# Performance work log

Hardware: AMD Instinct MI355X
Metric: run time of the kernel (lower is better)

## Reference

```python
import jax, jax.numpy as jnp
import numpy as np

B, C, H, W = 16, 512, 32, 32
HEADS = 8
GROUPS = 32
EPS = 1e-5


def setup_inputs() -> dict:
    key = jax.random.key(0)
    ks = jax.random.split(key, 6)
    x = jax.random.normal(ks[0], (B, C, H, W), dtype=jnp.float32)
    gn_scale = jnp.ones((C,), dtype=jnp.float32)
    gn_bias = jnp.zeros((C,), dtype=jnp.float32)
    # 1x1 convs stored as dense matrices [out, in]
    qkv_w = jax.random.normal(ks[1], (3 * C, C), dtype=jnp.float32) * (1.0 / np.sqrt(C))
    proj_w = jax.random.normal(ks[2], (C, C), dtype=jnp.float32) * (1.0 / np.sqrt(C))
    proj_b = jax.random.normal(ks[3], (C,), dtype=jnp.float32) * 0.01
    return {"x": x, "gn_scale": gn_scale, "gn_bias": gn_bias,
            "qkv_w": qkv_w, "proj_w": proj_w, "proj_b": proj_b}


def _forward(x, gn_scale, gn_bias, qkv_w, proj_w, proj_b):
    b, c, h, w = x.shape
    d = c // HEADS  # head dim
    n = h * w
    # GroupNorm over (channels_per_group, h, w)
    xg = x.reshape(b, GROUPS, c // GROUPS, h, w)
    mu = jnp.mean(xg, axis=(2, 3, 4), keepdims=True)
    var = jnp.var(xg, axis=(2, 3, 4), keepdims=True)
    xn = ((xg - mu) * jax.lax.rsqrt(var + EPS)).reshape(b, c, h, w)
    xn = xn * gn_scale[None, :, None, None] + gn_bias[None, :, None, None]
    # 1x1 conv QKV: [b, 3c, n]
    qkv = jnp.einsum('oc,bcn->bon', qkv_w, xn.reshape(b, c, n))
    # split order: (qkv, heads, d)
    qkv = qkv.reshape(b, 3, HEADS, d, n)
    q, k, v = qkv[:, 0], qkv[:, 1], qkv[:, 2]  # each [b, heads, d, n]
    k = jax.nn.softmax(k, axis=-1)
    att = jnp.einsum('bhdn,bhen->bhde', k, v)          # [b, heads, d, d]
    out = jnp.einsum('bhde,bhdn->bhen', att, q)        # [b, heads, d, n]
    out = out.reshape(b, c, h, w)
    # 1x1 proj conv with bias
    out = jnp.einsum('oc,bchw->bohw', proj_w, out) + proj_b[None, :, None, None]
    return out


def reference(x, gn_scale, gn_bias, qkv_w, proj_w, proj_b):
    return _forward(x, gn_scale, gn_bias, qkv_w, proj_w, proj_b)
```

## Files before the change

### kernel.cpp

```cpp
#include <hip/hip_runtime.h>
#include <cstdint>
#include <cstddef>

#define B_ 16
#define C_ 512
#define N_ 1024
#define HEADS_ 8
#define D_ 64
#define CPG_ 16

typedef __bf16 bf16;
typedef bf16 bf16x4 __attribute__((ext_vector_type(4)));
typedef bf16 bf16x8 __attribute__((ext_vector_type(8)));
typedef bf16 bf16x16 __attribute__((ext_vector_type(16)));
typedef float f32x4 __attribute__((ext_vector_type(4)));

__device__ __forceinline__ void gload16(void* lds, const void* g) {
    __builtin_amdgcn_global_load_lds(
        (__attribute__((address_space(1))) void*)(void*)g,
        (__attribute__((address_space(3))) void*)lds, 16, 0, 0);
}

__global__ __launch_bounds__(256) void f32_to_bf16_k(const float* __restrict__ s,
                                                     bf16* __restrict__ d, int n) {
    int i = (blockIdx.x * 256 + threadIdx.x) * 4;
    if (i < n) {
        f32x4 v = *(const f32x4*)(s + i);
        bf16x4 o = {(bf16)v[0], (bf16)v[1], (bf16)v[2], (bf16)v[3]};
        *(bf16x4*)(d + i) = o;
    }
}

__global__ __launch_bounds__(256) void gn_kernel(const float* __restrict__ x,
                                                 const float* __restrict__ gamma,
                                                 const float* __restrict__ beta,
                                                 bf16* __restrict__ xnT) {
    const int blk = blockIdx.x;
    const int b = blk >> 5, g = blk & 31;
    const int c0 = g * CPG_;
    const float* xb = x + ((size_t)b * C_ + c0) * N_;
    const int t = threadIdx.x;

    f32x4 vals[CPG_];
    float sum = 0.f, ssq = 0.f;
#pragma unroll
    for (int c = 0; c < CPG_; ++c) {
        f32x4 v = *(const f32x4*)(xb + c * N_ + t * 4);
        vals[c] = v;
#pragma unroll
        for (int j = 0; j < 4; ++j) { sum += v[j]; ssq += v[j] * v[j]; }
    }
#pragma unroll
    for (int off = 32; off >= 1; off >>= 1) {
        sum += __shfl_xor(sum, off);
        ssq += __shfl_xor(ssq, off);
    }
    __shared__ float red[2][4];
    const int wv = t >> 6, lane = t & 63;
    if (lane == 0) { red[0][wv] = sum; red[1][wv] = ssq; }
    __syncthreads();
    sum = red[0][0] + red[0][1] + red[0][2] + red[0][3];
    ssq = red[1][0] + red[1][1] + red[1][2] + red[1][3];
    const float inv = 1.f / (float)(CPG_ * N_);
    float mean = sum * inv;
    float var = ssq * inv - mean * mean;
    float rstd = rsqrtf(var + 1e-5f);
    float ga[CPG_], be[CPG_];
#pragma unroll
    for (int c = 0; c < CPG_; ++c) {
        float gm = gamma[c0 + c] * rstd;
        ga[c] = gm;
        be[c] = beta[c0 + c] - mean * gm;
    }
#pragma unroll
    for (int j = 0; j < 4; ++j) {
        int n = t * 4 + j;
        bf16x16 o;
#pragma unroll
        for (int c = 0; c < CPG_; ++c) o[c] = (bf16)(vals[c][j] * ga[c] + be[c]);
        *(bf16x16*)(xnT + ((size_t)b * N_ + n) * C_ + c0) = o;
    }
}

template <int EPI>
__global__ __launch_bounds__(256, 2) void gemm_bt(const bf16* __restrict__ A,
                                                  const bf16* __restrict__ Bt,
                                                  int M, int N, int K,
                                                  void* __restrict__ o0,
                                                  void* __restrict__ o1,
                                                  void* __restrict__ o2,
                                                  const float* __restrict__ bias) {
    __shared__ __align__(16) bf16 As[2][128][64];
    __shared__ __align__(16) bf16 Bs[2][128][64];
    const int t = threadIdx.x;
    const int lane = t & 63, wv = t >> 6;
    const int wr = wv >> 1, wc = wv & 1;
    const int bn = blockIdx.x, bm = blockIdx.y, b = blockIdx.z;
    const bf16* Ab = A + (size_t)bm * 128 * K;
    const bf16* Bb = Bt + ((size_t)b * N + (size_t)bn * 128) * K;

    f32x4 acc[4][4];
#pragma unroll
    for (int mi = 0; mi < 4; ++mi)
#pragma unroll
        for (int ni = 0; ni < 4; ++ni) acc[mi][ni] = f32x4{0.f, 0.f, 0.f, 0.f};

    const int nk = K >> 6;

    auto stage = [&](int buf, int kt) {
#pragma unroll
        for (int rnd = 0; rnd < 4; ++rnd) {
            int idx = rnd * 256 + t;
            int row = idx >> 3, pb = idx & 7;
            int srcb = pb ^ (row & 7);
            gload16((char*)&As[buf][0][0] + (size_t)idx * 16,
                    Ab + (size_t)row * K + kt * 64 + srcb * 8);
        }
#pragma unroll
        for (int rnd = 0; rnd < 4; ++rnd) {
            int idx = rnd * 256 + t;
            int row = idx >> 3, pb = idx & 7;
            int srcb = pb ^ (row & 7);
            gload16((char*)&Bs[buf][0][0] + (size_t)idx * 16,
                    Bb + (size_t)row * K + kt * 64 + srcb * 8);
        }
    };
    auto compute = [&](int buf) {
#pragma unroll
        for (int ks = 0; ks < 2; ++ks) {
            bf16x8 af[4], bfr[4];
#pragma unroll
            for (int mi = 0; mi < 4; ++mi) {
                int r = wr * 64 + mi * 16 + (lane & 15);
                int bi = (ks * 4 + (lane >> 4)) ^ (r & 7);
                af[mi] = *(const bf16x8*)&As[buf][r][bi * 8];
            }
#pragma unroll
            for (int ni = 0; ni < 4; ++ni) {
                int r = wc * 64 + ni * 16 + (lane & 15);
                int bi = (ks * 4 + (lane >> 4)) ^ (r & 7);
                bfr[ni] = *(const bf16x8*)&Bs[buf][r][bi * 8];
            }
#pragma unroll
            for (int mi = 0; mi < 4; ++mi)
#pragma unroll
                for (int ni = 0; ni < 4; ++ni)
                    acc[mi][ni] = __builtin_amdgcn_mfma_f32_16x16x32_bf16(
                        af[mi], bfr[ni], acc[mi][ni], 0, 0, 0);
        }
    };

    stage(0, 0);
    asm volatile("s_waitcnt vmcnt(0)" ::: "memory");
    __syncthreads();
    for (int kt = 0; kt < nk - 1; ++kt) {
        const int cur = kt & 1;
        stage(cur ^ 1, kt + 1);
        compute(cur);
        asm volatile("s_waitcnt vmcnt(0)" ::: "memory");
        __syncthreads();
    }
    compute((nk - 1) & 1);

    const int rowb = bm * 128 + wr * 64;
    const int colb = bn * 128 + wc * 64;
#pragma unroll
    for (int mi = 0; mi < 4; ++mi) {
#pragma unroll
        for (int ni = 0; ni < 4; ++ni) {
            int r0 = rowb + mi * 16 + (lane >> 4) * 4;
            int cc = colb + ni * 16 + (lane & 15);
            if constexpr (EPI == 0) {
                bf16* qT = (bf16*)o0;
                float* kf = (float*)o1;
                bf16* vb = (bf16*)o2;
                if (r0 < 512) {
                    int h = r0 >> 6, d = r0 & 63;
                    bf16x4 pk;
#pragma unroll
                    for (int j = 0; j < 4; ++j) pk[j] = (bf16)acc[mi][ni][j];
                    *(bf16x4*)(qT + (((size_t)b * HEADS_ + h) * N_ + cc) * D_ + d) = pk;
                } else if (r0 < 1024) {
                    int h = (r0 >> 6) - 8, d = r0 & 63;
                    float* kp = kf + (((size_t)b * HEADS_ + h) * D_ + d) * N_ + cc;
#pragma unroll
                    for (int j = 0; j < 4; ++j) kp[(size_t)j * N_] = acc[mi][ni][j];
                } else {
                    int h = (r0 >> 6) - 16, d = r0 & 63;
                    bf16* vp = vb + (((size_t)b * HEADS_ + h) * D_ + d) * N_ + cc;
#pragma unroll
                    for (int j = 0; j < 4; ++j) vp[(size_t)j * N_] = (bf16)acc[mi][ni][j];
                }
            } else {
                float* outp = (float*)o0;
#pragma unroll
                for (int j = 0; j < 4; ++j)
                    outp[((size_t)b * C_ + r0 + j) * N_ + cc] = acc[mi][ni][j] + bias[r0 + j];
            }
        }
    }
}

__global__ __launch_bounds__(256) void softmax_k(const float* __restrict__ kf,
                                                 bf16* __restrict__ ksm) {
    const int row = blockIdx.x * 4 + (threadIdx.x >> 6);
    const int lane = threadIdx.x & 63;
    const float* rp = kf + (size_t)row * N_;
    f32x4 v[4];
    float mx = -1e30f;
#pragma unroll
    for (int i = 0; i < 4; ++i) {
        v[i] = *(const f32x4*)(rp + (lane + 64 * i) * 4);
#pragma unroll
        for (int j = 0; j < 4; ++j) mx = fmaxf(mx, v[i][j]);
    }
#pragma unroll
    for (int off = 32; off >= 1; off >>= 1) mx = fmaxf(mx, __shfl_xor(mx, off));
    float s = 0.f;
#pragma unroll
    for (int i = 0; i < 4; ++i)
#pragma unroll
        for (int j = 0; j < 4; ++j) { v[i][j] = __expf(v[i][j] - mx); s += v[i][j]; }
#pragma unroll
    for (int off = 32; off >= 1; off >>= 1) s += __shfl_xor(s, off);
    float inv = 1.f / s;
    bf16* op = ksm + (size_t)row * N_;
#pragma unroll
    for (int i = 0; i < 4; ++i) {
        bf16x4 o;
#pragma unroll
        for (int j = 0; j < 4; ++j) o[j] = (bf16)(v[i][j] * inv);
        *(bf16x4*)(op + (lane + 64 * i) * 4) = o;
    }
}

__global__ __launch_bounds__(256) void attn_kernel(const bf16* __restrict__ ksm,
                                                   const bf16* __restrict__ vb,
                                                   const bf16* __restrict__ qT,
                                                   bf16* __restrict__ o2T) {
    __shared__ float attp[2][64][64];
    __shared__ __align__(16) bf16 attT[64][64];
    const int bh = blockIdx.x;
    const int b = bh >> 3, h = bh & 7;
    const int t = threadIdx.x, lane = t & 63, wv = t >> 6;
    const bf16* kb = ksm + (size_t)bh * D_ * N_;
    const bf16* vv = vb + (size_t)bh * D_ * N_;
    const bf16* qb = qT + (size_t)bh * N_ * D_;

    f32x4 acc[4][4];
#pragma unroll
    for (int mi = 0; mi < 4; ++mi)
#pragma unroll
        for (int ni = 0; ni < 4; ++ni) acc[mi][ni] = f32x4{0.f, 0.f, 0.f, 0.f};

    const int k0 = wv * 256;
    for (int kk = 0; kk < 256; kk += 32) {
        bf16x8 af[4], bfr[4];
#pragma unroll
        for (int mi = 0; mi < 4; ++mi)
            af[mi] = *(const bf16x8*)(kb + (size_t)(mi * 16 + (lane & 15)) * N_ + k0 + kk + (lane >> 4) * 8);
#pragma unroll
        for (int ni = 0; ni < 4; ++ni)
            bfr[ni] = *(const bf16x8*)(vv + (size_t)(ni * 16 + (lane & 15)) * N_ + k0 + kk + (lane >> 4) * 8);
#pragma unroll
        for (int mi = 0; mi < 4; ++mi)
#pragma unroll
            for (int ni = 0; ni < 4; ++ni)
                acc[mi][ni] = __builtin_amdgcn_mfma_f32_16x16x32_bf16(
                    af[mi], bfr[ni], acc[mi][ni], 0, 0, 0);
    }
    if (wv < 2) {
#pragma unroll
        for (int mi = 0; mi < 4; ++mi)
#pragma unroll
            for (int ni = 0; ni < 4; ++ni)
#pragma unroll
                for (int j = 0; j < 4; ++j)
                    attp[wv][mi * 16 + (lane >> 4) * 4 + j][ni * 16 + (lane & 15)] = acc[mi][ni][j];
    }
    __syncthreads();
    if (wv >= 2) {
#pragma unroll
        for (int mi = 0; mi < 4; ++mi)
#pragma unroll
            for (int ni = 0; ni < 4; ++ni)
#pragma unroll
                for (int j = 0; j < 4; ++j)
                    attp[wv - 2][mi * 16 + (lane >> 4) * 4 + j][ni * 16 + (lane & 15)] += acc[mi][ni][j];
    }
    __syncthreads();
    for (int i = t; i < 4096; i += 256) {
        int d = i >> 6, e = i & 63;
        float s = attp[0][d][e] + attp[1][d][e];
        attT[e][d ^ ((e & 7) << 3)] = (bf16)s;
    }
    __syncthreads();

    for (int nc = 0; nc < 4; ++nc) {
        int n0 = wv * 256 + nc * 64;
        f32x4 a2[4][4];
#pragma unroll
        for (int mi = 0; mi < 4; ++mi)
#pragma unroll
            for (int ni = 0; ni < 4; ++ni) a2[mi][ni] = f32x4{0.f, 0.f, 0.f, 0.f};
#pragma unroll
        for (int ks = 0; ks < 2; ++ks) {
            bf16x8 af[4], bfr[4];
#pragma unroll
            for (int mi = 0; mi < 4; ++mi) {
                int r = mi * 16 + (lane & 15);
                int cb = ks * 32 + (lane >> 4) * 8;
                af[mi] = *(const bf16x8*)&attT[r][cb ^ ((r & 7) << 3)];
            }
#pragma unroll
            for (int ni = 0; ni < 4; ++ni)
                bfr[ni] = *(const bf16x8*)(qb + (size_t)(n0 + ni * 16 + (lane & 15)) * D_ + ks * 32 + (lane >> 4) * 8);
#pragma unroll
            for (int mi = 0; mi < 4; ++mi)
#pragma unroll
                for (int ni = 0; ni < 4; ++ni)
                    a2[mi][ni] = __builtin_amdgcn_mfma_f32_16x16x32_bf16(
                        af[mi], bfr[ni], a2[mi][ni], 0, 0, 0);
        }
#pragma unroll
        for (int mi = 0; mi < 4; ++mi) {
#pragma unroll
            for (int ni = 0; ni < 4; ++ni) {
                int e0 = mi * 16 + (lane >> 4) * 4;
                int nn = n0 + ni * 16 + (lane & 15);
                bf16x4 pk;
#pragma unroll
                for (int j = 0; j < 4; ++j) pk[j] = (bf16)a2[mi][ni][j];
                *(bf16x4*)(o2T + ((size_t)b * N_ + nn) * C_ + h * D_ + e0) = pk;
            }
        }
    }
}

extern "C" void kernel_launch(void* const* d_in, const int* in_sizes, int n_in,
                              void* d_out, int out_size, void* d_ws, size_t ws_size,
                              hipStream_t stream) {
    const float* x = (const float*)d_in[0];
    const float* gn_scale = (const float*)d_in[1];
    const float* gn_bias = (const float*)d_in[2];
    const float* qkv_w = (const float*)d_in[3];
    const float* proj_w = (const float*)d_in[4];
    const float* proj_b = (const float*)d_in[5];
    float* out = (float*)d_out;

    const size_t elems = (size_t)B_ * C_ * N_;
    char* w = (char*)d_ws;
    bf16* xnT = (bf16*)w;   w += elems * 2;
    bf16* qT = (bf16*)w;    w += (size_t)B_ * HEADS_ * N_ * D_ * 2;
    float* kf = (float*)w;  w += (size_t)B_ * HEADS_ * D_ * N_ * 4;
    bf16* ksm = (bf16*)w;   w += (size_t)B_ * HEADS_ * D_ * N_ * 2;
    bf16* vbuf = (bf16*)w;  w += (size_t)B_ * HEADS_ * D_ * N_ * 2;
    bf16* wqkv = (bf16*)w;  w += (size_t)3 * C_ * C_ * 2;
    bf16* wproj = (bf16*)w; w += (size_t)C_ * C_ * 2;
    bf16* o2T = xnT;

    f32_to_bf16_k<<<768, 256, 0, stream>>>(qkv_w, wqkv, 3 * C_ * C_);
    f32_to_bf16_k<<<256, 256, 0, stream>>>(proj_w, wproj, C_ * C_);
    gn_kernel<<<512, 256, 0, stream>>>(x, gn_scale, gn_bias, xnT);
    gemm_bt<0><<<dim3(8, 12, 16), 256, 0, stream>>>(wqkv, xnT, 1536, 1024, 512,
                                                    (void*)qT, (void*)kf, (void*)vbuf, nullptr);
    softmax_k<<<2048, 256, 0, stream>>>(kf, ksm);
    attn_kernel<<<128, 256, 0, stream>>>(ksm, vbuf, qT, o2T);
    gemm_bt<1><<<dim3(8, 4, 16), 256, 0, stream>>>(wproj, o2T, 512, 1024, 512,
                                                   (void*)out, nullptr, nullptr, proj_b);
}
```

Before: 188.0 us.

## Split attention into two wider kernels, store K logits in bf16, relax GEMM waits

The single 128-block attention kernel is split in two. The first computes partial K·V^T over half the sequence across 256 blocks and writes fp32 partials. The second sums the partials and multiplies by Q across 512 blocks, which should fill more CUs on the MI355X. K logits are now written in bf16 rather than fp32, halving that buffer's traffic into softmax at some cost in precision before the exponent. The GEMM main loop waits with vmcnt(8) instead of a full drain and uses raw barriers, so the next tile's loads can overlap compute; it also adds an extra workspace buffer and an extra launch.

New measurement: 181.6 us. 1.04x faster.

```diff
diff --git a/kernel.cpp b/kernel.cpp
--- a/kernel.cpp
+++ b/kernel.cpp
@@ -151,16 +151,19 @@
     };
 
     stage(0, 0);
-    asm volatile("s_waitcnt vmcnt(0)" ::: "memory");
-    __syncthreads();
-    for (int kt = 0; kt < nk - 1; ++kt) {
+    for (int kt = 0; kt < nk; ++kt) {
         const int cur = kt & 1;
-        stage(cur ^ 1, kt + 1);
+        if (kt + 1 < nk) {
+            stage(cur ^ 1, kt + 1);
+            asm volatile("s_waitcnt vmcnt(8)" ::: "memory");
+        } else {
+            asm volatile("s_waitcnt vmcnt(0)" ::: "memory");
+        }
+        __builtin_amdgcn_s_barrier();
+        __builtin_amdgcn_sched_barrier(0);
         compute(cur);
-        asm volatile("s_waitcnt vmcnt(0)" ::: "memory");
-        __syncthreads();
-    }
-    compute((nk - 1) & 1);
+        __builtin_amdgcn_s_barrier();
+    }
 
     const int rowb = bm * 128 + wr * 64;
     const int colb = bn * 128 + wc * 64;
@@ -172,7 +175,7 @@
             int cc = colb + ni * 16 + (lane & 15);
             if constexpr (EPI == 0) {
                 bf16* qT = (bf16*)o0;
-                float* kf = (float*)o1;
+                bf16* klog = (bf16*)o1;
                 bf16* vb = (bf16*)o2;
                 if (r0 < 512) {
                     int h = r0 >> 6, d = r0 & 63;
@@ -180,16 +183,12 @@
 #pragma unroll
                     for (int j = 0; j < 4; ++j) pk[j] = (bf16)acc[mi][ni][j];
                     *(bf16x4*)(qT + (((size_t)b * HEADS_ + h) * N_ + cc) * D_ + d) = pk;
-                } else if (r0 < 1024) {
-                    int h = (r0 >> 6) - 8, d = r0 & 63;
-                    float* kp = kf + (((size_t)b * HEADS_ + h) * D_ + d) * N_ + cc;
-#pragma unroll
-                    for (int j = 0; j < 4; ++j) kp[(size_t)j * N_] = acc[mi][ni][j];
                 } else {
-                    int h = (r0 >> 6) - 16, d = r0 & 63;
-                    bf16* vp = vb + (((size_t)b * HEADS_ + h) * D_ + d) * N_ + cc;
-#pragma unroll
-                    for (int j = 0; j < 4; ++j) vp[(size_t)j * N_] = (bf16)acc[mi][ni][j];
+                    bf16* dst = (r0 < 1024) ? klog : vb;
+                    int h = (r0 >> 6) & 7, d = r0 & 63;
+                    bf16* p = dst + (((size_t)b * HEADS_ + h) * D_ + d) * N_ + cc;
+#pragma unroll
+                    for (int j = 0; j < 4; ++j) p[(size_t)j * N_] = (bf16)acc[mi][ni][j];
                 }
             } else {
                 float* outp = (float*)o0;
@@ -201,51 +200,49 @@
     }
 }
 
-__global__ __launch_bounds__(256) void softmax_k(const float* __restrict__ kf,
+__global__ __launch_bounds__(256) void softmax_k(const bf16* __restrict__ klog,
                                                  bf16* __restrict__ ksm) {
     const int row = blockIdx.x * 4 + (threadIdx.x >> 6);
     const int lane = threadIdx.x & 63;
-    const float* rp = kf + (size_t)row * N_;
-    f32x4 v[4];
+    const bf16* rp = klog + (size_t)row * N_;
+    float v[16];
     float mx = -1e30f;
 #pragma unroll
-    for (int i = 0; i < 4; ++i) {
-        v[i] = *(const f32x4*)(rp + (lane + 64 * i) * 4);
-#pragma unroll
-        for (int j = 0; j < 4; ++j) mx = fmaxf(mx, v[i][j]);
+    for (int i = 0; i < 2; ++i) {
+        bf16x8 u = *(const bf16x8*)(rp + ((size_t)lane + 64 * i) * 8);
+#pragma unroll
+        for (int j = 0; j < 8; ++j) {
+            v[i * 8 + j] = (float)u[j];
+            mx = fmaxf(mx, v[i * 8 + j]);
+        }
     }
 #pragma unroll
     for (int off = 32; off >= 1; off >>= 1) mx = fmaxf(mx, __shfl_xor(mx, off));
     float s = 0.f;
 #pragma unroll
-    for (int i = 0; i < 4; ++i)
-#pragma unroll
-        for (int j = 0; j < 4; ++j) { v[i][j] = __expf(v[i][j] - mx); s += v[i][j]; }
+    for (int i = 0; i < 16; ++i) { v[i] = __expf(v[i] - mx); s += v[i]; }
 #pragma unroll
     for (int off = 32; off >= 1; off >>= 1) s += __shfl_xor(s, off);
     float inv = 1.f / s;
     bf16* op = ksm + (size_t)row * N_;
 #pragma unroll
-    for (int i = 0; i < 4; ++i) {
-        bf16x4 o;
-#pragma unroll
-        for (int j = 0; j < 4; ++j) o[j] = (bf16)(v[i][j] * inv);
-        *(bf16x4*)(op + (lane + 64 * i) * 4) = o;
-    }
-}
-
-__global__ __launch_bounds__(256) void attn_kernel(const bf16* __restrict__ ksm,
-                                                   const bf16* __restrict__ vb,
-                                                   const bf16* __restrict__ qT,
-                                                   bf16* __restrict__ o2T) {
+    for (int i = 0; i < 2; ++i) {
+        bf16x8 o;
+#pragma unroll
+        for (int j = 0; j < 8; ++j) o[j] = (bf16)(v[i * 8 + j] * inv);
+        *(bf16x8*)(op + ((size_t)lane + 64 * i) * 8) = o;
+    }
+}
+
+__global__ __launch_bounds__(256) void attn1_kernel(const bf16* __restrict__ ksm,
+                                                    const bf16* __restrict__ vb,
+                                                    float* __restrict__ attP) {
     __shared__ float attp[2][64][64];
-    __shared__ __align__(16) bf16 attT[64][64];
-    const int bh = blockIdx.x;
-    const int b = bh >> 3, h = bh & 7;
+    const int blk = blockIdx.x;
+    const int bh = blk >> 1, half = blk & 1;
     const int t = threadIdx.x, lane = t & 63, wv = t >> 6;
     const bf16* kb = ksm + (size_t)bh * D_ * N_;
     const bf16* vv = vb + (size_t)bh * D_ * N_;
-    const bf16* qb = qT + (size_t)bh * N_ * D_;
 
     f32x4 acc[4][4];
 #pragma unroll
@@ -253,8 +250,9 @@
 #pragma unroll
         for (int ni = 0; ni < 4; ++ni) acc[mi][ni] = f32x4{0.f, 0.f, 0.f, 0.f};
 
-    const int k0 = wv * 256;
-    for (int kk = 0; kk < 256; kk += 32) {
+    const int k0 = half * 512 + wv * 128;
+#pragma unroll
+    for (int kk = 0; kk < 128; kk += 32) {
         bf16x8 af[4], bfr[4];
 #pragma unroll
         for (int mi = 0; mi < 4; ++mi)
@@ -289,50 +287,65 @@
                     attp[wv - 2][mi * 16 + (lane >> 4) * 4 + j][ni * 16 + (lane & 15)] += acc[mi][ni][j];
     }
     __syncthreads();
+    float* op = attP + (size_t)blk * 4096;
     for (int i = t; i < 4096; i += 256) {
         int d = i >> 6, e = i & 63;
-        float s = attp[0][d][e] + attp[1][d][e];
-        attT[e][d ^ ((e & 7) << 3)] = (bf16)s;
+        op[i] = attp[0][d][e] + attp[1][d][e];
+    }
+}
+
+__global__ __launch_bounds__(256) void attn2_kernel(const float* __restrict__ attP,
+                                                    const bf16* __restrict__ qT,
+                                                    bf16* __restrict__ o2T) {
+    __shared__ __align__(16) bf16 attT[64][64];
+    const int blk = blockIdx.x;
+    const int bh = blk >> 2, nc = blk & 3;
+    const int b = bh >> 3, h = bh & 7;
+    const int t = threadIdx.x, lane = t & 63, wv = t >> 6;
+    const float* p0 = attP + (size_t)(bh * 2) * 4096;
+    const float* p1 = p0 + 4096;
+    for (int i = t; i < 4096; i += 256) {
+        int d = i >> 6, e = i & 63;
+        attT[e][d ^ ((e & 7) << 3)] = (bf16)(p0[i] + p1[i]);
     }
     __syncthreads();
 
-    for (int nc = 0; nc < 4; ++nc) {
-        int n0 = wv * 256 + nc * 64;
-        f32x4 a2[4][4];
-#pragma unroll
-        for (int mi = 0; mi < 4; ++mi)
-#pragma unroll
-            for (int ni = 0; ni < 4; ++ni) a2[mi][ni] = f32x4{0.f, 0.f, 0.f, 0.f};
-#pragma unroll
-        for (int ks = 0; ks < 2; ++ks) {
-            bf16x8 af[4], bfr[4];
-#pragma unroll
-            for (int mi = 0; mi < 4; ++mi) {
-                int r = mi * 16 + (lane & 15);
-                int cb = ks * 32 + (lane >> 4) * 8;
-                af[mi] = *(const bf16x8*)&attT[r][cb ^ ((r & 7) << 3)];
-            }
+    const bf16* qb = qT + (size_t)bh * N_ * D_;
+    const int n0 = nc * 256 + wv * 64;
+    f32x4 a2[4][4];
+#pragma unroll
+    for (int mi = 0; mi < 4; ++mi)
+#pragma unroll
+        for (int ni = 0; ni < 4; ++ni) a2[mi][ni] = f32x4{0.f, 0.f, 0.f, 0.f};
+#pragma unroll
+    for (int ks = 0; ks < 2; ++ks) {
+        bf16x8 af[4], bfr[4];
+#pragma unroll
+        for (int mi = 0; mi < 4; ++mi) {
+            int r = mi * 16 + (lane & 15);
+            int cb = ks * 32 + (lane >> 4) * 8;
+            af[mi] = *(const bf16x8*)&attT[r][cb ^ ((r & 7) << 3)];
+        }
+#pragma unroll
+        for (int ni = 0; ni < 4; ++ni)
+            bfr[ni] = *(const bf16x8*)(qb + (size_t)(n0 + ni * 16 + (lane & 15)) * D_ + ks * 32 + (lane >> 4) * 8);
+#pragma unroll
+        for (int mi = 0; mi < 4; ++mi)
 #pragma unroll
             for (int ni = 0; ni < 4; ++ni)
-                bfr[ni] = *(const bf16x8*)(qb + (size_t)(n0 + ni * 16 + (lane & 15)) * D_ + ks * 32 + (lane >> 4) * 8);
-#pragma unroll
-            for (int mi = 0; mi < 4; ++mi)
-#pragma unroll
-                for (int ni = 0; ni < 4; ++ni)
-                    a2[mi][ni] = __builtin_amdgcn_mfma_f32_16x16x32_bf16(
-                        af[mi], bfr[ni], a2[mi][ni], 0, 0, 0);
-        }
-#pragma unroll
-        for (int mi = 0; mi < 4; ++mi) {
-#pragma unroll
-            for (int ni = 0; ni < 4; ++ni) {
-                int e0 = mi * 16 + (lane >> 4) * 4;
-                int nn = n0 + ni * 16 + (lane & 15);
-                bf16x4 pk;
-#pragma unroll
-                for (int j = 0; j < 4; ++j) pk[j] = (bf16)a2[mi][ni][j];
-                *(bf16x4*)(o2T + ((size_t)b * N_ + nn) * C_ + h * D_ + e0) = pk;
-            }
+                a2[mi][ni] = __builtin_amdgcn_mfma_f32_16x16x32_bf16(
+                    af[mi], bfr[ni], a2[mi][ni], 0, 0, 0);
+    }
+#pragma unroll
+    for (int mi = 0; mi < 4; ++mi) {
+#pragma unroll
+        for (int ni = 0; ni < 4; ++ni) {
+            int e0 = mi * 16 + (lane >> 4) * 4;
+            int nn = n0 + ni * 16 + (lane & 15);
+            bf16x4 pk;
+#pragma unroll
+            for (int j = 0; j < 4; ++j) pk[j] = (bf16)a2[mi][ni][j];
+            *(bf16x4*)(o2T + ((size_t)b * N_ + nn) * C_ + h * D_ + e0) = pk;
         }
     }
 }
@@ -349,12 +362,14 @@
     float* out = (float*)d_out;
 
     const size_t elems = (size_t)B_ * C_ * N_;
+    const size_t plane = (size_t)B_ * HEADS_ * D_ * N_;
     char* w = (char*)d_ws;
     bf16* xnT = (bf16*)w;   w += elems * 2;
-    bf16* qT = (bf16*)w;    w += (size_t)B_ * HEADS_ * N_ * D_ * 2;
-    float* kf = (float*)w;  w += (size_t)B_ * HEADS_ * D_ * N_ * 4;
-    bf16* ksm = (bf16*)w;   w += (size_t)B_ * HEADS_ * D_ * N_ * 2;
-    bf16* vbuf = (bf16*)w;  w += (size_t)B_ * HEADS_ * D_ * N_ * 2;
+    bf16* qT = (bf16*)w;    w += plane * 2;
+    bf16* klog = (bf16*)w;  w += plane * 2;
+    bf16* ksm = (bf16*)w;   w += plane * 2;
+    bf16* vbuf = (bf16*)w;  w += plane * 2;
+    float* attP = (float*)w; w += (size_t)256 * 4096 * 4;
     bf16* wqkv = (bf16*)w;  w += (size_t)3 * C_ * C_ * 2;
     bf16* wproj = (bf16*)w; w += (size_t)C_ * C_ * 2;
     bf16* o2T = xnT;
@@ -363,9 +378,10 @@
     f32_to_bf16_k<<<256, 256, 0, stream>>>(proj_w, wproj, C_ * C_);
     gn_kernel<<<512, 256, 0, stream>>>(x, gn_scale, gn_bias, xnT);
     gemm_bt<0><<<dim3(8, 12, 16), 256, 0, stream>>>(wqkv, xnT, 1536, 1024, 512,
-                                                    (void*)qT, (void*)kf, (void*)vbuf, nullptr);
-    softmax_k<<<2048, 256, 0, stream>>>(kf, ksm);
-    attn_kernel<<<128, 256, 0, stream>>>(ksm, vbuf, qT, o2T);
+                                                    (void*)qT, (void*)klog, (void*)vbuf, nullptr);
+    softmax_k<<<2048, 256, 0, stream>>>(klog, ksm);
+    attn1_kernel<<<256, 256, 0, stream>>>(ksm, vbuf, attP);
+    attn2_kernel<<<512, 256, 0, stream>>>(attP, qT, o2T);
     gemm_bt<1><<<dim3(8, 4, 16), 256, 0, stream>>>(wproj, o2T, 512, 1024, 512,
                                                    (void*)out, nullptr, nullptr, proj_b);
 }
```
